# Kernel tuning notes

Measured on AMD Instinct MI355X. Metric: run time of the kernel, lower is better.

## Reference

```python
import jax, jax.numpy as jnp
import numpy as np

HEADS = 16

def setup_inputs() -> dict:
    key = jax.random.key(0)
    ks = jax.random.split(key, 8)
    B, Lq, G, Lkv, dim, dim_kv = 4, 512, 4, 1024, 1024, 1024
    inner = dim_kv  # dim_per_head * heads = (dim_kv // heads) * heads
    H = jax.random.normal(ks[0], (B, Lq, dim), dtype=jnp.float32)
    KV = jax.random.normal(ks[1], (B, G, Lkv, dim_kv), dtype=jnp.float32)
    KV_mask = jax.random.randint(ks[2], (B, G, Lkv), 0, 2, dtype=jnp.int32)
    s = 0.02
    Wq = jax.random.normal(ks[3], (dim, inner), dtype=jnp.float32) * s
    Wk = jax.random.normal(ks[4], (dim_kv, inner), dtype=jnp.float32) * s
    Wv = jax.random.normal(ks[5], (dim_kv, inner), dtype=jnp.float32) * s
    Wo = jax.random.normal(ks[6], (inner, dim), dtype=jnp.float32) * s
    return {"H": H, "KV": KV, "KV_mask": KV_mask,
            "Wq": Wq, "Wk": Wk, "Wv": Wv, "Wo": Wo}


def reference(H, KV, KV_mask, Wq, Wk, Wv, Wo):
    B, Lq, dim = H.shape
    _, G, Lkv, dim_kv = KV.shape
    inner = Wq.shape[1]
    h = HEADS
    d = inner // h

    # q: [B, h, Lq, d], pre-scaled as in the torch module
    q = (H @ Wq).reshape(B, Lq, h, d).transpose(0, 2, 1, 3) * (d ** -0.5)
    # k, v: [B, G, h, Lkv, d] -- all graphs batched instead of Python loop
    k = jnp.einsum('bgle,ef->bglf', KV, Wk).reshape(B, G, Lkv, h, d).transpose(0, 1, 3, 2, 4)
    v = jnp.einsum('bgle,ef->bglf', KV, Wv).reshape(B, G, Lkv, h, d).transpose(0, 1, 3, 2, 4)

    # scores: [B, G, h, Lq, Lkv]
    scores = jnp.einsum('bhqd,bghkd->bghqk', q, k)
    # additive mask: (1 - mask) * finfo.min, mask broadcast over heads & queries
    mask = KV_mask.astype(scores.dtype)  # [B, G, Lkv]
    scores = scores + (1.0 - mask)[:, :, None, None, :] * jnp.finfo(scores.dtype).min

    attn = jax.nn.softmax(scores.astype(jnp.float32), axis=-1).astype(scores.dtype)
    ctx = jnp.einsum('bghqk,bghkd->bghqd', attn, v)  # [B, G, h, Lq, d]
    ctx = ctx.transpose(0, 1, 3, 2, 4).reshape(B, G, Lq, inner)
    out = ctx @ Wo  # [B, G, Lq, dim]
    # concat over graphs along last dim, matching torch.cat(all_attn, dim=-1)
    out = out.transpose(0, 2, 1, 3).reshape(B, Lq, G * dim)
    return out
```

## Files before the change

kernel.cpp:

```cpp
#include <hip/hip_runtime.h>

using f16   = _Float16;
using f16x8 = _Float16 __attribute__((ext_vector_type(8)));
using f16x4 = _Float16 __attribute__((ext_vector_type(4)));
using f32x4 = float    __attribute__((ext_vector_type(4)));

constexpr int BM = 128, BN = 128, BK = 64;
constexpr int KD = 1024, ND = 1024;

__device__ __forceinline__ int swz(int r, int c) {
  return r * BK + ((c ^ (r & 7)) << 3);
}

__device__ __forceinline__ void gload_lds16(const f16* g, f16* s) {
  __builtin_amdgcn_global_load_lds(
      (const __attribute__((address_space(1))) void*)g,
      (__attribute__((address_space(3))) void*)s, 16, 0, 0);
}

__device__ __forceinline__ int2 xcd_swz() {
  int lin = blockIdx.y * gridDim.x + blockIdx.x;
  int per = (gridDim.x * gridDim.y) >> 3;
  int sw  = (lin & 7) * per + (lin >> 3);
  return make_int2(sw % gridDim.x, sw / gridDim.x);
}

__global__ __launch_bounds__(256)
void cast_k(const float* __restrict__ in, f16* __restrict__ out) {
  size_t i = ((size_t)blockIdx.x * 256 + threadIdx.x) * 8;
  f32x4 a = *(const f32x4*)(in + i);
  f32x4 b = *(const f32x4*)(in + i + 4);
  f16x8 o;
  o[0] = (f16)a[0]; o[1] = (f16)a[1]; o[2] = (f16)a[2]; o[3] = (f16)a[3];
  o[4] = (f16)b[0]; o[5] = (f16)b[1]; o[6] = (f16)b[2]; o[7] = (f16)b[3];
  *(f16x8*)(out + i) = o;
}

__global__ __launch_bounds__(256)
void wtrans_k(const float* __restrict__ W, f16* __restrict__ Wt) {
  __shared__ float tile[32][33];
  int bx = blockIdx.x * 32;
  int by = blockIdx.y * 32;
  int tx = threadIdx.x, ty = threadIdx.y;
#pragma unroll
  for (int i = 0; i < 4; ++i) {
    int r = ty + i * 8;
    tile[r][tx] = W[(size_t)(by + r) * ND + bx + tx];
  }
  __syncthreads();
#pragma unroll
  for (int i = 0; i < 4; ++i) {
    int r = ty + i * 8;
    Wt[(size_t)(bx + r) * KD + by + tx] = (f16)tile[tx][r];
  }
}

template <int MODE>
__global__ __launch_bounds__(256)
void gemm_k(const f16* __restrict__ A, const f16* __restrict__ Bt,
            void* __restrict__ C, float scale) {
  __shared__ __attribute__((aligned(16))) f16 As[BM * BK];
  __shared__ __attribute__((aligned(16))) f16 Bs[BN * BK];
  const int t = threadIdx.x;
  const int w = t >> 6, l = t & 63, l15 = l & 15, lg = l >> 4;
  const int2 bi = xcd_swz();
  const int m0 = bi.y * BM, n0 = bi.x * BN;
  const int wm = (w >> 1) * 64, wn = (w & 1) * 64;
  const int lr  = l >> 3;
  const int csw = ((l & 7) ^ lr) << 3;

  const f16* Ab = A  + (size_t)m0 * KD + csw;
  const f16* Bb = Bt + (size_t)n0 * KD + csw;

  f32x4 acc[4][4] = {};

  for (int kb = 0; kb < KD; kb += BK) {
#pragma unroll
    for (int i = 0; i < 4; ++i) {
      int ii = w * 4 + i;
      int r  = ii * 8 + lr;
      gload_lds16(Ab + (size_t)r * KD + kb, &As[ii * 512]);
      gload_lds16(Bb + (size_t)r * KD + kb, &Bs[ii * 512]);
    }
    __syncthreads();
#pragma unroll
    for (int ks = 0; ks < 2; ++ks) {
      f16x8 av[4], bw[4];
      int cc = ks * 4 + lg;
#pragma unroll
      for (int mf = 0; mf < 4; ++mf)
        av[mf] = *(const f16x8*)&As[swz(wm + mf * 16 + l15, cc)];
#pragma unroll
      for (int nf = 0; nf < 4; ++nf)
        bw[nf] = *(const f16x8*)&Bs[swz(wn + nf * 16 + l15, cc)];
#pragma unroll
      for (int mf = 0; mf < 4; ++mf)
#pragma unroll
        for (int nf = 0; nf < 4; ++nf)
          acc[mf][nf] = __builtin_amdgcn_mfma_f32_16x16x32_f16(
              av[mf], bw[nf], acc[mf][nf], 0, 0, 0);
    }
    __syncthreads();
  }

#pragma unroll
  for (int mf = 0; mf < 4; ++mf) {
#pragma unroll
    for (int nf = 0; nf < 4; ++nf) {
      int mb = m0 + wm + mf * 16 + 4 * lg;
      int n  = n0 + wn + nf * 16 + l15;
      if (MODE == 0) {
#pragma unroll
        for (int r = 0; r < 4; ++r)
          ((f16*)C)[(size_t)(mb + r) * ND + n] = (f16)(acc[mf][nf][r] * scale);
      } else if (MODE == 1) {
        int bg = mb >> 10, kv = mb & 1023;
        int h = n >> 6, e = n & 63;
        f16x4 pk;
#pragma unroll
        for (int r = 0; r < 4; ++r) pk[r] = (f16)acc[mf][nf][r];
        *(f16x4*)((f16*)C + (size_t)((bg * 16 + h) * 64 + e) * 1024 + kv) = pk;
      } else {
#pragma unroll
        for (int r = 0; r < 4; ++r) {
          int m = mb + r;
          int bg = m >> 9, lq = m & 511;
          int bb = bg >> 2, g = bg & 3;
          ((float*)C)[(size_t)(((bb << 9) + lq) * 4 + g) * 1024 + n] =
              acc[mf][nf][r];
        }
      }
    }
  }
}

__global__ __launch_bounds__(256)
void attn_k(const f16* __restrict__ Qb, const f16* __restrict__ Kb,
            const f16* __restrict__ Vt, const int* __restrict__ mask,
            f16* __restrict__ ctx) {
  __shared__ int smask[1024];
  __shared__ __attribute__((aligned(16))) f16 Ks[2][64 * 64];
  __shared__ __attribute__((aligned(16))) f16 Vs[2][64 * 64];
  __shared__ __attribute__((aligned(16))) f16 Pl[4][16 * 72];

  const int t = threadIdx.x, w = t >> 6, l = t & 63, l15 = l & 15, lg = l >> 4;
  const int y = blockIdx.y, bg = y >> 4, h = y & 15, bb = bg >> 2;
  const int q0 = blockIdx.x * 128 + w * 32;
  const int lr = l >> 3, csw = ((l & 7) ^ lr) << 3;

  *(int4*)&smask[t * 4] = *(const int4*)(mask + bg * 1024 + t * 4);

  f16x8 aQ[2][2];
#pragma unroll
  for (int mf = 0; mf < 2; ++mf) {
    const f16* qp =
        Qb + (size_t)(bb * 512 + q0 + mf * 16 + l15) * 1024 + h * 64 + lg * 8;
    aQ[mf][0] = *(const f16x8*)qp;
    aQ[mf][1] = *(const f16x8*)(qp + 32);
  }

  float mrow[2][4], rs[2][4];
#pragma unroll
  for (int mf = 0; mf < 2; ++mf)
#pragma unroll
    for (int r = 0; r < 4; ++r) { mrow[mf][r] = -1e30f; rs[mf][r] = 0.f; }
  f32x4 accO[2][4] = {};

  const f16* Kbase = Kb + (size_t)bg * (1024 * 1024) + h * 64 + csw;
  const f16* Vbase = Vt + (size_t)(bg * 16 + h) * (64 * 1024) + csw;

  auto stage = [&](int tile, int buf) {
    const int kv0 = tile * 64;
#pragma unroll
    for (int i = 0; i < 2; ++i) {
      int ii = w * 2 + i;
      int r  = ii * 8 + lr;
      gload_lds16(Kbase + (size_t)(kv0 + r) * 1024, &Ks[buf][ii * 512]);
      gload_lds16(Vbase + (size_t)r * 1024 + kv0,   &Vs[buf][ii * 512]);
    }
  };

  __syncthreads();
  stage(0, 0);

  for (int c16 = 0; c16 < 16; ++c16) {
    const int cur = c16 & 1;
    const int kv0 = c16 * 64;
    if (c16 < 15) {
      stage(c16 + 1, cur ^ 1);
      asm volatile("s_waitcnt vmcnt(4)" ::: "memory");
    } else {
      asm volatile("s_waitcnt vmcnt(0)" ::: "memory");
    }
    __builtin_amdgcn_s_barrier();
    __builtin_amdgcn_sched_barrier(0);

    f32x4 s[2][4] = {};
    __builtin_amdgcn_s_setprio(1);
#pragma unroll
    for (int nf = 0; nf < 4; ++nf) {
      int kr = nf * 16 + l15;
      f16x8 k0 = *(const f16x8*)&Ks[cur][swz(kr, lg)];
      f16x8 k1 = *(const f16x8*)&Ks[cur][swz(kr, 4 + lg)];
#pragma unroll
      for (int mf = 0; mf < 2; ++mf) {
        s[mf][nf] = __builtin_amdgcn_mfma_f32_16x16x32_f16(aQ[mf][0], k0, s[mf][nf], 0, 0, 0);
        s[mf][nf] = __builtin_amdgcn_mfma_f32_16x16x32_f16(aQ[mf][1], k1, s[mf][nf], 0, 0, 0);
      }
    }
    __builtin_amdgcn_s_setprio(0);
#pragma unroll
    for (int nf = 0; nf < 4; ++nf) {
      if (smask[kv0 + nf * 16 + l15] == 0) {
#pragma unroll
        for (int mf = 0; mf < 2; ++mf)
#pragma unroll
          for (int r = 0; r < 4; ++r) s[mf][nf][r] = -1e30f;
      }
    }
    f16x8 bV[2][4];
#pragma unroll
    for (int ks = 0; ks < 2; ++ks)
#pragma unroll
      for (int nf = 0; nf < 4; ++nf)
        bV[ks][nf] = *(const f16x8*)&Vs[cur][swz(nf * 16 + l15, ks * 4 + lg)];

#pragma unroll
    for (int mf = 0; mf < 2; ++mf) {
#pragma unroll
      for (int r = 0; r < 4; ++r) {
        float v = fmaxf(fmaxf(s[mf][0][r], s[mf][1][r]),
                        fmaxf(s[mf][2][r], s[mf][3][r]));
        v = fmaxf(v, __shfl_xor(v, 1));
        v = fmaxf(v, __shfl_xor(v, 2));
        v = fmaxf(v, __shfl_xor(v, 4));
        v = fmaxf(v, __shfl_xor(v, 8));
        float mn = mrow[mf][r];
        if (v > mn + 8.f) {
          float sc = __expf(mn - v);
          mn = v; mrow[mf][r] = v;
          rs[mf][r] *= sc;
#pragma unroll
          for (int nf = 0; nf < 4; ++nf) accO[mf][nf][r] *= sc;
        }
        float ps = 0.f;
#pragma unroll
        for (int nf = 0; nf < 4; ++nf) {
          float p = __expf(s[mf][nf][r] - mn);
          ps += p;
          Pl[w][(4 * lg + r) * 72 + nf * 16 + l15] = (f16)p;
        }
        rs[mf][r] += ps;
      }
      __builtin_amdgcn_s_setprio(1);
#pragma unroll
      for (int ks = 0; ks < 2; ++ks) {
        f16x8 aP = *(const f16x8*)&Pl[w][l15 * 72 + ks * 32 + lg * 8];
#pragma unroll
        for (int nf = 0; nf < 4; ++nf)
          accO[mf][nf] = __builtin_amdgcn_mfma_f32_16x16x32_f16(aP, bV[ks][nf], accO[mf][nf], 0, 0, 0);
      }
      __builtin_amdgcn_s_setprio(0);
    }

    asm volatile("s_waitcnt lgkmcnt(0)" ::: "memory");
    __builtin_amdgcn_s_barrier();
  }

#pragma unroll
  for (int mf = 0; mf < 2; ++mf)
#pragma unroll
    for (int r = 0; r < 4; ++r) {
      float v = rs[mf][r];
      v += __shfl_xor(v, 1);
      v += __shfl_xor(v, 2);
      v += __shfl_xor(v, 4);
      v += __shfl_xor(v, 8);
      rs[mf][r] = 1.0f / v;
    }
#pragma unroll
  for (int mf = 0; mf < 2; ++mf)
#pragma unroll
    for (int nf = 0; nf < 4; ++nf)
#pragma unroll
      for (int r = 0; r < 4; ++r) {
        int q = q0 + mf * 16 + 4 * lg + r;
        ctx[(size_t)(bg * 512 + q) * 1024 + h * 64 + nf * 16 + l15] =
            (f16)(accO[mf][nf][r] * rs[mf][r]);
      }
}

extern "C" void kernel_launch(void* const* d_in, const int* in_sizes, int n_in,
                              void* d_out, int out_size, void* d_ws,
                              size_t ws_size, hipStream_t stream) {
  const float* H  = (const float*)d_in[0];
  const float* KV = (const float*)d_in[1];
  const int*  msk = (const int*)d_in[2];
  const float* Wq = (const float*)d_in[3];
  const float* Wk = (const float*)d_in[4];
  const float* Wv = (const float*)d_in[5];
  const float* Wo = (const float*)d_in[6];

  char* ws = (char*)d_ws;
  f16* WqT  = (f16*)(ws + ((size_t)0  << 20));
  f16* WkT  = (f16*)(ws + ((size_t)2  << 20));
  f16* WvT  = (f16*)(ws + ((size_t)4  << 20));
  f16* WoT  = (f16*)(ws + ((size_t)6  << 20));
  f16* Hf   = (f16*)(ws + ((size_t)8  << 20));
  f16* KVf  = (f16*)(ws + ((size_t)12 << 20));
  f16* Qb   = (f16*)(ws + ((size_t)12 << 20));
  f16* ctxf = (f16*)(ws + ((size_t)16 << 20));
  f16* Kb   = (f16*)(ws + ((size_t)44 << 20));
  f16* Vtb  = (f16*)(ws + ((size_t)76 << 20));

  cast_k<<<1024, 256, 0, stream>>>(H,  Hf);
  cast_k<<<8192, 256, 0, stream>>>(KV, KVf);

  dim3 tb32(32, 8);
  wtrans_k<<<dim3(32, 32), tb32, 0, stream>>>(Wq, WqT);
  wtrans_k<<<dim3(32, 32), tb32, 0, stream>>>(Wk, WkT);
  wtrans_k<<<dim3(32, 32), tb32, 0, stream>>>(Wv, WvT);
  wtrans_k<<<dim3(32, 32), tb32, 0, stream>>>(Wo, WoT);

  gemm_k<0><<<dim3(8, 128), 256, 0, stream>>>(KVf, WkT, (void*)Kb,  1.0f);
  gemm_k<1><<<dim3(8, 128), 256, 0, stream>>>(KVf, WvT, (void*)Vtb, 1.0f);
  gemm_k<0><<<dim3(8, 16),  256, 0, stream>>>(Hf,  WqT, (void*)Qb,  0.125f);

  attn_k<<<dim3(4, 256), 256, 0, stream>>>(Qb, Kb, Vtb, msk, ctxf);

  gemm_k<2><<<dim3(8, 64), 256, 0, stream>>>(ctxf, WoT, d_out, 1.0f);
}
```

Baseline: 386.2 us.

## Load K and V fragments directly from global memory, dropping LDS double buffering

```diff
diff --git a/kernel.cpp b/kernel.cpp
--- a/kernel.cpp
+++ b/kernel.cpp
@@ -139,16 +139,14 @@
             const f16* __restrict__ Vt, const int* __restrict__ mask,
             f16* __restrict__ ctx) {
   __shared__ int smask[1024];
-  __shared__ __attribute__((aligned(16))) f16 Ks[2][64 * 64];
-  __shared__ __attribute__((aligned(16))) f16 Vs[2][64 * 64];
-  __shared__ __attribute__((aligned(16))) f16 Pl[4][16 * 72];
+  __shared__ __attribute__((aligned(16))) f16 Pl[4][32 * 72];
 
   const int t = threadIdx.x, w = t >> 6, l = t & 63, l15 = l & 15, lg = l >> 4;
   const int y = blockIdx.y, bg = y >> 4, h = y & 15, bb = bg >> 2;
   const int q0 = blockIdx.x * 128 + w * 32;
-  const int lr = l >> 3, csw = ((l & 7) ^ lr) << 3;
 
   *(int4*)&smask[t * 4] = *(const int4*)(mask + bg * 1024 + t * 4);
+  __syncthreads();
 
   f16x8 aQ[2][2];
 #pragma unroll
@@ -166,49 +164,32 @@
     for (int r = 0; r < 4; ++r) { mrow[mf][r] = -1e30f; rs[mf][r] = 0.f; }
   f32x4 accO[2][4] = {};
 
-  const f16* Kbase = Kb + (size_t)bg * (1024 * 1024) + h * 64 + csw;
-  const f16* Vbase = Vt + (size_t)(bg * 16 + h) * (64 * 1024) + csw;
-
-  auto stage = [&](int tile, int buf) {
-    const int kv0 = tile * 64;
-#pragma unroll
-    for (int i = 0; i < 2; ++i) {
-      int ii = w * 2 + i;
-      int r  = ii * 8 + lr;
-      gload_lds16(Kbase + (size_t)(kv0 + r) * 1024, &Ks[buf][ii * 512]);
-      gload_lds16(Vbase + (size_t)r * 1024 + kv0,   &Vs[buf][ii * 512]);
-    }
-  };
-
-  __syncthreads();
-  stage(0, 0);
+  const f16* Kh = Kb + (size_t)bg * (1024 * 1024) + h * 64;
+  const f16* Vh = Vt + (size_t)(bg * 16 + h) * (64 * 1024);
 
   for (int c16 = 0; c16 < 16; ++c16) {
-    const int cur = c16 & 1;
     const int kv0 = c16 * 64;
-    if (c16 < 15) {
-      stage(c16 + 1, cur ^ 1);
-      asm volatile("s_waitcnt vmcnt(4)" ::: "memory");
-    } else {
-      asm volatile("s_waitcnt vmcnt(0)" ::: "memory");
-    }
-    __builtin_amdgcn_s_barrier();
-    __builtin_amdgcn_sched_barrier(0);
+
+    f16x8 k0[4], k1[4];
+#pragma unroll
+    for (int nf = 0; nf < 4; ++nf) {
+      const f16* kp = Kh + (size_t)(kv0 + nf * 16 + l15) * 1024 + lg * 8;
+      k0[nf] = *(const f16x8*)kp;
+      k1[nf] = *(const f16x8*)(kp + 32);
+    }
 
     f32x4 s[2][4] = {};
     __builtin_amdgcn_s_setprio(1);
 #pragma unroll
     for (int nf = 0; nf < 4; ++nf) {
-      int kr = nf * 16 + l15;
-      f16x8 k0 = *(const f16x8*)&Ks[cur][swz(kr, lg)];
-      f16x8 k1 = *(const f16x8*)&Ks[cur][swz(kr, 4 + lg)];
 #pragma unroll
       for (int mf = 0; mf < 2; ++mf) {
-        s[mf][nf] = __builtin_amdgcn_mfma_f32_16x16x32_f16(aQ[mf][0], k0, s[mf][nf], 0, 0, 0);
-        s[mf][nf] = __builtin_amdgcn_mfma_f32_16x16x32_f16(aQ[mf][1], k1, s[mf][nf], 0, 0, 0);
+        s[mf][nf] = __builtin_amdgcn_mfma_f32_16x16x32_f16(aQ[mf][0], k0[nf], s[mf][nf], 0, 0, 0);
+        s[mf][nf] = __builtin_amdgcn_mfma_f32_16x16x32_f16(aQ[mf][1], k1[nf], s[mf][nf], 0, 0, 0);
       }
     }
     __builtin_amdgcn_s_setprio(0);
+
 #pragma unroll
     for (int nf = 0; nf < 4; ++nf) {
       if (smask[kv0 + nf * 16 + l15] == 0) {
@@ -218,12 +199,6 @@
           for (int r = 0; r < 4; ++r) s[mf][nf][r] = -1e30f;
       }
     }
-    f16x8 bV[2][4];
-#pragma unroll
-    for (int ks = 0; ks < 2; ++ks)
-#pragma unroll
-      for (int nf = 0; nf < 4; ++nf)
-        bV[ks][nf] = *(const f16x8*)&Vs[cur][swz(nf * 16 + l15, ks * 4 + lg)];
 
 #pragma unroll
     for (int mf = 0; mf < 2; ++mf) {
@@ -248,23 +223,29 @@
         for (int nf = 0; nf < 4; ++nf) {
           float p = __expf(s[mf][nf][r] - mn);
           ps += p;
-          Pl[w][(4 * lg + r) * 72 + nf * 16 + l15] = (f16)p;
+          Pl[w][(mf * 16 + 4 * lg + r) * 72 + nf * 16 + l15] = (f16)p;
         }
         rs[mf][r] += ps;
       }
-      __builtin_amdgcn_s_setprio(1);
-#pragma unroll
-      for (int ks = 0; ks < 2; ++ks) {
-        f16x8 aP = *(const f16x8*)&Pl[w][l15 * 72 + ks * 32 + lg * 8];
-#pragma unroll
-        for (int nf = 0; nf < 4; ++nf)
-          accO[mf][nf] = __builtin_amdgcn_mfma_f32_16x16x32_f16(aP, bV[ks][nf], accO[mf][nf], 0, 0, 0);
-      }
-      __builtin_amdgcn_s_setprio(0);
-    }
-
-    asm volatile("s_waitcnt lgkmcnt(0)" ::: "memory");
-    __builtin_amdgcn_s_barrier();
+    }
+
+    __builtin_amdgcn_s_setprio(1);
+#pragma unroll
+    for (int ks = 0; ks < 2; ++ks) {
+      f16x8 bV[4];
+#pragma unroll
+      for (int nf = 0; nf < 4; ++nf)
+        bV[nf] = *(const f16x8*)(Vh + (size_t)(nf * 16 + l15) * 1024 + kv0 +
+                                 ks * 32 + lg * 8);
+      f16x8 aP0 = *(const f16x8*)&Pl[w][l15 * 72 + ks * 32 + lg * 8];
+      f16x8 aP1 = *(const f16x8*)&Pl[w][(16 + l15) * 72 + ks * 32 + lg * 8];
+#pragma unroll
+      for (int nf = 0; nf < 4; ++nf) {
+        accO[0][nf] = __builtin_amdgcn_mfma_f32_16x16x32_f16(aP0, bV[nf], accO[0][nf], 0, 0, 0);
+        accO[1][nf] = __builtin_amdgcn_mfma_f32_16x16x32_f16(aP1, bV[nf], accO[1][nf], 0, 0, 0);
+      }
+    }
+    __builtin_amdgcn_s_setprio(0);
   }
 
 #pragma unroll
```

Measured after the change: 412.6 us. 6.8% more time.
